# Kernel tuning notes

Hardware: AMD Instinct MI355X
Metric: run time of the kernel (lower is better)

The kernel has to match this reference:

```python
import jax, jax.numpy as jnp
import numpy as np

VOCAB = 8192
NT = 10        # spike encoder n_timesteps
N = 2048       # n_neurons
CA3 = 2048     # hippocampus CA3 size
S = 1024       # seq_len / context_length
SPARSITY = 0.05
LR = 0.01      # learning_rate * association_strength


def setup_inputs() -> dict:
    key = jax.random.key(0)
    k1, k2, k3, k4, k5 = jax.random.split(key, 5)
    token_ids = jax.random.randint(k1, (1, S), 0, VOCAB)                      # [batch=1, seq]
    sdr_table = jax.random.uniform(k2, (VOCAB, NT, N), dtype=jnp.float32)     # SDR encoder table
    pos_enc = jax.random.uniform(k3, (S, NT, N), dtype=jnp.float32)           # oscillatory position spikes (pre-threshold)
    w_hippo = jax.random.normal(k4, (CA3, N), dtype=jnp.float32) / np.sqrt(N).astype(np.float32)
    assoc_w = jax.random.normal(k5, (CA3, CA3), dtype=jnp.float32) * 0.01     # WEIGHT_INIT_SCALE_RECURRENT gaussian
    return {"token_ids": token_ids, "sdr_table": sdr_table, "pos_enc": pos_enc,
            "w_hippo": w_hippo, "assoc_w": assoc_w}


def reference(token_ids, sdr_table, pos_enc, w_hippo, assoc_w):
    """encode_sequence(learn=True): spike-encode each token, modulate by position
    spikes, run hippocampus, and sequentially Hebbian-update association weights.
    Returns final association weight matrix [CA3, CA3]."""
    tok_spikes = (sdr_table[token_ids[0]] < SPARSITY).astype(jnp.float32)
    # Position spikes (as_spikes=True -> binary) -> [S, NT, N]
    pos_spikes = (pos_enc < SPARSITY).astype(jnp.float32)
    # combined_spikes = token * (1 + 0.5 * position); sum over timesteps -> [S, N]
    hippo_input = (tok_spikes * (1.0 + 0.5 * pos_spikes)).sum(axis=1)
    # Hippocampus CA3 spikes: linear projection + threshold -> binary pattern [S, CA3]
    ca3_patterns = (hippo_input @ w_hippo.T > 0.0).astype(jnp.float32)

    # Sequential Hebbian association learning: W += lr * outer(post, pre), row-renorm.
    def step(W, pre_post):
        pre, post = pre_post
        W = W + LR * jnp.outer(post, pre)
        norm = jnp.maximum(jnp.linalg.norm(W, axis=1, keepdims=True), 1.0)
        return W / norm, None

    W_final, _ = jax.lax.scan(step, assoc_w, (ca3_patterns[:-1], ca3_patterns[1:]))
    return W_final
```

## Files before the change

### kernel.cpp

```cpp
#include <hip/hip_runtime.h>
#include <hip/hip_bf16.h>

#define NT    10
#define NN    2048
#define CA3C  2048
#define SEQ   1024
#define SPARS 0.05f
#define LRC   0.01f

typedef float          f32x4  __attribute__((ext_vector_type(4)));
typedef short          bf16x8 __attribute__((ext_vector_type(8)));
typedef unsigned short u16x4  __attribute__((ext_vector_type(4)));
typedef unsigned short u16x8  __attribute__((ext_vector_type(8)));

__device__ __forceinline__ unsigned short f2bf(float f) {
    unsigned u = __float_as_uint(f);
    u += 0x7FFFu + ((u >> 16) & 1u);
    return (unsigned short)(u >> 16);
}
__device__ __forceinline__ float bf2f(unsigned short h) {
    return __uint_as_float(((unsigned)h) << 16);
}

__device__ __forceinline__ void split8(const float* __restrict__ src,
        unsigned short* __restrict__ hi, unsigned short* __restrict__ lo, long blk) {
    long i = (blk * 256 + threadIdx.x) * 8;
    f32x4 x0 = *(const f32x4*)(src + i);
    f32x4 x1 = *(const f32x4*)(src + i + 4);
    float xs[8] = {x0.x, x0.y, x0.z, x0.w, x1.x, x1.y, x1.z, x1.w};
    u16x8 h, l;
    #pragma unroll
    for (int j = 0; j < 8; ++j) {
        unsigned short hb = f2bf(xs[j]);
        h[j] = hb;
        l[j] = f2bf(xs[j] - bf2f(hb));
    }
    *(u16x8*)(hi + i) = h;
    if (lo) *(u16x8*)(lo + i) = l;
}

__global__ __launch_bounds__(256) void k_front(const int* __restrict__ tok,
        const float* __restrict__ sdr, const float* __restrict__ pos,
        unsigned short* __restrict__ Hh, unsigned* __restrict__ cnt,
        const float* __restrict__ w_hippo, unsigned short* __restrict__ Wh,
        unsigned short* __restrict__ Wl, const float* __restrict__ assoc,
        unsigned short* __restrict__ Sh) {
    long id = blockIdx.x;
    if (id == 0 && threadIdx.x == 0) *cnt = 0;
    if (id < 2048) {
        int s = (int)(id >> 1);
        int n = ((int)(id & 1) * 256 + threadIdx.x) * 4;
        const float* sp = sdr + (long)tok[s] * (NT * NN) + n;
        const float* pp = pos + (long)s * (NT * NN) + n;
        float a0 = 0.f, a1 = 0.f, a2 = 0.f, a3 = 0.f;
        #pragma unroll
        for (int t = 0; t < NT; ++t) {
            float4 sv = *(const float4*)(sp + t * NN);
            float4 pv = *(const float4*)(pp + t * NN);
            if (sv.x < SPARS) a0 += (pv.x < SPARS) ? 1.5f : 1.0f;
            if (sv.y < SPARS) a1 += (pv.y < SPARS) ? 1.5f : 1.0f;
            if (sv.z < SPARS) a2 += (pv.z < SPARS) ? 1.5f : 1.0f;
            if (sv.w < SPARS) a3 += (pv.w < SPARS) ? 1.5f : 1.0f;
        }
        u16x4 o = { f2bf(a0), f2bf(a1), f2bf(a2), f2bf(a3) };
        *(u16x4*)(Hh + (long)s * NN + n) = o;
    } else {
        long b = id - 2048;
        if (b < 2048) split8(w_hippo, Wh, Wl, b);
        else          split8(assoc, Sh, nullptr, b - 2048);
    }
}

#define SPLIT_NONE 0
#define SPLIT_A    1
#define SPLIT_B    2

template<int MODE, int BN>
__global__ __launch_bounds__(256, 1) void k_mgemm(
        const unsigned short* __restrict__ A0, const unsigned short* __restrict__ A1,
        const unsigned short* __restrict__ Bh, const unsigned short* __restrict__ B1,
        float* __restrict__ C, int M, int N, int K,
        const float* __restrict__ Wadd, const float* __restrict__ af) {
    constexpr int NTW = BN / 32;
    constexpr int XR  = (MODE == SPLIT_A) ? 128 : BN;
    __shared__ unsigned short LA[128 * 70];
    __shared__ unsigned short LB[BN * 70];
    __shared__ unsigned short LX[(MODE == SPLIT_NONE) ? 70 : XR * 70];
    int tid = threadIdx.x, wid = tid >> 6, l = tid & 63;
    int m0 = blockIdx.y * 128, n0 = blockIdx.x * BN;
    int wr = wid >> 1, wc = wid & 1;
    int fr = l & 15, fk = l >> 4;
    f32x4 acc[4][NTW] = {};
    int srow = wid * 8 + (l >> 3);
    int scol = (l & 7) * 8;
    bf16x8 ra[4], rb[BN / 32], rx[XR / 32];
    #pragma unroll
    for (int i = 0; i < 4; ++i)
        ra[i] = *(const bf16x8*)(A0 + (long)(m0 + i * 32 + srow) * K + scol);
    #pragma unroll
    for (int i = 0; i < BN / 32; ++i)
        rb[i] = *(const bf16x8*)(Bh + (long)(n0 + i * 32 + srow) * K + scol);
    if (MODE == SPLIT_A)
        #pragma unroll
        for (int i = 0; i < XR / 32; ++i)
            rx[i] = *(const bf16x8*)(A1 + (long)(m0 + i * 32 + srow) * K + scol);
    if (MODE == SPLIT_B)
        #pragma unroll
        for (int i = 0; i < XR / 32; ++i)
            rx[i] = *(const bf16x8*)(B1 + (long)(n0 + i * 32 + srow) * K + scol);

    for (int k0 = 0; k0 < K; k0 += 64) {
        __syncthreads();
        #pragma unroll
        for (int i = 0; i < 4; ++i) *(bf16x8*)&LA[(i * 32 + srow) * 70 + scol] = ra[i];
        #pragma unroll
        for (int i = 0; i < BN / 32; ++i) *(bf16x8*)&LB[(i * 32 + srow) * 70 + scol] = rb[i];
        if (MODE != SPLIT_NONE)
            #pragma unroll
            for (int i = 0; i < XR / 32; ++i) *(bf16x8*)&LX[(i * 32 + srow) * 70 + scol] = rx[i];
        __syncthreads();
        if (k0 + 64 < K) {
            int kn = k0 + 64;
            #pragma unroll
            for (int i = 0; i < 4; ++i)
                ra[i] = *(const bf16x8*)(A0 + (long)(m0 + i * 32 + srow) * K + kn + scol);
            #pragma unroll
            for (int i = 0; i < BN / 32; ++i)
                rb[i] = *(const bf16x8*)(Bh + (long)(n0 + i * 32 + srow) * K + kn + scol);
            if (MODE == SPLIT_A)
                #pragma unroll
                for (int i = 0; i < XR / 32; ++i)
                    rx[i] = *(const bf16x8*)(A1 + (long)(m0 + i * 32 + srow) * K + kn + scol);
            if (MODE == SPLIT_B)
                #pragma unroll
                for (int i = 0; i < XR / 32; ++i)
                    rx[i] = *(const bf16x8*)(B1 + (long)(n0 + i * 32 + srow) * K + kn + scol);
        }
        #pragma unroll
        for (int ks = 0; ks < 2; ++ks) {
            bf16x8 av[4], bv[NTW], xv[4];
            #pragma unroll
            for (int t = 0; t < 4; ++t)
                av[t] = *(const bf16x8*)&LA[(wr * 64 + t * 16 + fr) * 70 + ks * 32 + fk * 8];
            #pragma unroll
            for (int t = 0; t < NTW; ++t)
                bv[t] = *(const bf16x8*)&LB[(wc * (BN / 2) + t * 16 + fr) * 70 + ks * 32 + fk * 8];
            if (MODE == SPLIT_A)
                #pragma unroll
                for (int t = 0; t < 4; ++t)
                    xv[t] = *(const bf16x8*)&LX[(wr * 64 + t * 16 + fr) * 70 + ks * 32 + fk * 8];
            if (MODE == SPLIT_B)
                #pragma unroll
                for (int t = 0; t < NTW; ++t)
                    xv[t] = *(const bf16x8*)&LX[(wc * (BN / 2) + t * 16 + fr) * 70 + ks * 32 + fk * 8];
            #pragma unroll
            for (int mt = 0; mt < 4; ++mt)
                #pragma unroll
                for (int nt = 0; nt < NTW; ++nt) {
                    acc[mt][nt] = __builtin_amdgcn_mfma_f32_16x16x32_bf16(av[mt], bv[nt], acc[mt][nt], 0, 0, 0);
                    if (MODE == SPLIT_A)
                        acc[mt][nt] = __builtin_amdgcn_mfma_f32_16x16x32_bf16(xv[mt], bv[nt], acc[mt][nt], 0, 0, 0);
                    if (MODE == SPLIT_B)
                        acc[mt][nt] = __builtin_amdgcn_mfma_f32_16x16x32_bf16(av[mt], xv[nt], acc[mt][nt], 0, 0, 0);
                }
        }
    }
    int drb = (l >> 4) * 4;
    #pragma unroll
    for (int mt = 0; mt < 4; ++mt)
        #pragma unroll
        for (int nt = 0; nt < NTW; ++nt)
            #pragma unroll
            for (int e = 0; e < 4; ++e) {
                int row = m0 + wr * 64 + mt * 16 + drb + e;
                int cc  = n0 + wc * (BN / 2) + nt * 16 + (l & 15);
                float v = acc[mt][nt][e];
                if (Wadd) v = fmaf(af[row], Wadd[(long)row * N + cc], v);
                C[(long)row * N + cc] = v;
            }
}

__global__ __launch_bounds__(256) void k_fixflag(const float* __restrict__ dots,
        unsigned* __restrict__ list, unsigned* __restrict__ cnt) {
    int i = blockIdx.x * 256 + threadIdx.x;
    int lane = threadIdx.x & 63;
    bool f = fabsf(dots[i]) < 1e-3f;
    unsigned long long m = __ballot(f);
    if (m == 0) return;
    unsigned b0 = 0;
    if (lane == 0) b0 = atomicAdd(cnt, (unsigned)__popcll(m));
    b0 = __shfl(b0, 0, 64);
    if (f) {
        unsigned rank = (unsigned)__popcll(m & ((1ull << lane) - 1ull));
        list[b0 + rank] = (unsigned)i;
    }
}

__global__ __launch_bounds__(64) void k_fix64(const unsigned* __restrict__ list,
        const unsigned* __restrict__ cnt, const unsigned short* __restrict__ Hh,
        const float* __restrict__ w, float* __restrict__ dots) {
    int lane = threadIdx.x;
    unsigned n = *cnt;
    for (unsigned idx = blockIdx.x; idx < n; idx += gridDim.x) {
        unsigned i = list[idx];
        int s = (int)(i >> 11), c = (int)(i & 2047);
        const unsigned short* hr = Hh + (long)s * NN;
        const float* wr = w + (long)c * NN;
        double a = 0.0;
        #pragma unroll
        for (int j = 0; j < 8; ++j) {
            int k = j * 256 + lane * 4;
            f32x4 wv = *(const f32x4*)(wr + k);
            u16x4 hv = *(const u16x4*)(hr + k);
            a += (double)bf2f(hv.x) * (double)wv.x + (double)bf2f(hv.y) * (double)wv.y
               + (double)bf2f(hv.z) * (double)wv.z + (double)bf2f(hv.w) * (double)wv.w;
        }
        #pragma unroll
        for (int o = 1; o < 64; o <<= 1) a += __shfl_xor(a, o, 64);
        if (lane == 0) dots[i] = (a > 0.0) ? 1.0f : -1.0f;
    }
}

__global__ __launch_bounds__(256) void k_packx(const float* __restrict__ dots,
        unsigned* __restrict__ preT, float* __restrict__ popf,
        unsigned short* __restrict__ Xb, unsigned* __restrict__ postT) {
    int wid = threadIdx.x >> 6, lane = threadIdx.x & 63;
    if (blockIdx.x < 256) {
        int s = blockIdx.x * 4 + wid;
        const float* row = dots + (long)s * CA3C + lane * 32;
        unsigned short* xrow = Xb + (long)s * CA3C + lane * 32;
        unsigned m = 0;
        #pragma unroll
        for (int j4 = 0; j4 < 8; ++j4) {
            f32x4 v = *(const f32x4*)(row + j4 * 4);
            u16x4 xb;
            xb.x = v.x > 0.f ? 0x3F80 : 0; xb.y = v.y > 0.f ? 0x3F80 : 0;
            xb.z = v.z > 0.f ? 0x3F80 : 0; xb.w = v.w > 0.f ? 0x3F80 : 0;
            m |= (v.x > 0.f ? 1u : 0u) << (j4 * 4 + 0);
            m |= (v.y > 0.f ? 1u : 0u) << (j4 * 4 + 1);
            m |= (v.z > 0.f ? 1u : 0u) << (j4 * 4 + 2);
            m |= (v.w > 0.f ? 1u : 0u) << (j4 * 4 + 3);
            *(u16x4*)(xrow + j4 * 4) = xb;
        }
        preT[lane * SEQ + s] = m;
        int pc = __popc(m);
        #pragma unroll
        for (int o = 1; o < 64; o <<= 1) pc += __shfl_xor(pc, o, 64);
        if (lane == 0) popf[s] = (float)pc;
    } else {
        __shared__ unsigned long long masks[4][64];
        int tile = (blockIdx.x - 256) * 4 + wid;
        int rg = tile & 31, sg = tile >> 5;
        int r0 = rg * 64;
        #pragma unroll 8
        for (int k = 0; k < 64; ++k) {
            int s = sg * 64 + k;
            float d = (s < SEQ - 1) ? dots[(long)(s + 1) * CA3C + r0 + lane] : -1.f;
            unsigned long long m = __ballot(d > 0.f);
            if (lane == 0) masks[wid][k] = m;
        }
        unsigned w0 = 0, w1 = 0;
        #pragma unroll
        for (int k = 0; k < 32; ++k) {
            w0 |= (unsigned)((masks[wid][k]      >> lane) & 1ull) << k;
            w1 |= (unsigned)((masks[wid][k + 32] >> lane) & 1ull) << k;
        }
        postT[(r0 + lane) * 32 + sg * 2]     = w0;
        postT[(r0 + lane) * 32 + sg * 2 + 1] = w1;
    }
}

__global__ __launch_bounds__(256) void k_transpose(const unsigned short* __restrict__ Xb,
        unsigned short* __restrict__ XbT) {
    __shared__ unsigned short t[64][72];
    int s0 = blockIdx.x * 64, n0 = blockIdx.y * 64;
    int tx = threadIdx.x & 63, ty = threadIdx.x >> 6;
    #pragma unroll
    for (int ii = 0; ii < 16; ++ii) {
        int i = ty + ii * 4;
        t[i][tx] = Xb[(long)(s0 + i) * CA3C + n0 + tx];
    }
    __syncthreads();
    #pragma unroll
    for (int ii = 0; ii < 16; ++ii) {
        int i = ty + ii * 4;
        XbT[(long)(n0 + i) * SEQ + s0 + tx] = t[tx][i];
    }
}

__global__ __launch_bounds__(256) void k_gram(const unsigned* __restrict__ preT,
        float* __restrict__ G, unsigned short* __restrict__ Gbh,
        unsigned short* __restrict__ Gbl) {
    int i = blockIdx.x;
    int t = threadIdx.x;
    int a0 = 0, a1 = 0, a2 = 0, a3 = 0;
    #pragma unroll 8
    for (int w = 0; w < 64; ++w) {
        unsigned ri = preT[w * SEQ + i];
        const unsigned* pr = preT + w * SEQ;
        a0 += __popc(ri & pr[t]);
        a1 += __popc(ri & pr[t + 256]);
        a2 += __popc(ri & pr[t + 512]);
        a3 += __popc(ri & pr[t + 768]);
    }
    long base = (long)i * SEQ;
    int vi[4] = {a0, a1, a2, a3};
    #pragma unroll
    for (int q = 0; q < 4; ++q) {
        long o = base + t + q * 256;
        float v = (float)vi[q];
        unsigned short h = f2bf(v);
        G[o] = v;
        Gbh[o] = h;
        Gbl[o] = f2bf(v - bf2f(h));
    }
}

__device__ __forceinline__ float wave_sum64(float x) {
    #define DPPADD(ctrl, rmask) \
        x += __int_as_float(__builtin_amdgcn_update_dpp(0, __float_as_int(x), ctrl, rmask, 0xF, true))
    DPPADD(0xB1, 0xF);
    DPPADD(0x4E, 0xF);
    DPPADD(0x141, 0xF);
    DPPADD(0x140, 0xF);
    DPPADD(0x142, 0xA);
    DPPADD(0x143, 0xC);
    #undef DPPADD
    return __int_as_float(__builtin_amdgcn_readlane(__float_as_int(x), 63));
}

__global__ __launch_bounds__(256) void k_scan2(const float* __restrict__ W0,
        const float* __restrict__ B0, const float* __restrict__ G,
        const unsigned short* __restrict__ Gbh, const unsigned short* __restrict__ Gbl,
        const unsigned* __restrict__ postT, const float* __restrict__ popf,
        unsigned short* __restrict__ Ch, unsigned short* __restrict__ Cl,
        float* __restrict__ alphaf) {
    __shared__ float Gd[64][68];
    __shared__ unsigned short BH[2][4096];
    __shared__ unsigned short BL[2][4096];
    __shared__ unsigned short CHL[8][1024];
    int tid = threadIdx.x, wid = tid >> 6, lane = tid & 63;
    int r = blockIdx.x * 4 + wid;
    int fr = lane & 15, fk = lane >> 4;
    int nl = tid >> 2, seg = tid & 3;
    const float* wr = W0 + (long)r * NN + lane * 32;
    f32x4 q0 = *(const f32x4*)(wr +  0), q1 = *(const f32x4*)(wr +  4);
    f32x4 q2 = *(const f32x4*)(wr +  8), q3 = *(const f32x4*)(wr + 12);
    f32x4 q4 = *(const f32x4*)(wr + 16), q5 = *(const f32x4*)(wr + 20);
    f32x4 q6 = *(const f32x4*)(wr + 24), q7 = *(const f32x4*)(wr + 28);
    f32x4 pp = q0*q0 + q1*q1 + q2*q2 + q3*q3 + q4*q4 + q5*q5 + q6*q6 + q7*q7;
    float nu = wave_sum64((pp.x + pp.y) + (pp.z + pp.w));
    float alpha = 1.f, inv_alpha = 1.f;
    { float t = fmaxf(nu, 1.f); alpha *= rsqrtf(t); inv_alpha *= sqrtf(t); nu = fminf(nu, 1.f); }
    float s0 = 1.f;

    bf16x8 ph0, ph1, pl0, pl1;
    for (int b = 0; b < 16; ++b) {
        __syncthreads();
        {
            const float* gs = G + (long)(b * 64 + nl) * SEQ + b * 64 + seg * 16;
            *(f32x4*)&Gd[nl][seg * 16 +  0] = *(const f32x4*)(gs +  0);
            *(f32x4*)&Gd[nl][seg * 16 +  4] = *(const f32x4*)(gs +  4);
            *(f32x4*)&Gd[nl][seg * 16 +  8] = *(const f32x4*)(gs +  8);
            *(f32x4*)&Gd[nl][seg * 16 + 12] = *(const f32x4*)(gs + 12);
        }
        if (b > 0) {
            const unsigned short* gh = Gbh + (long)(b * 64 + nl) * SEQ + seg * 16;
            const unsigned short* gl = Gbl + (long)(b * 64 + nl) * SEQ + seg * 16;
            ph0 = *(const bf16x8*)(gh); ph1 = *(const bf16x8*)(gh + 8);
            pl0 = *(const bf16x8*)(gl); pl1 = *(const bf16x8*)(gl + 8);
            *(bf16x8*)&BH[0][((seg * 2 + 0) * 64 + nl) * 8] = ph0;
            *(bf16x8*)&BH[0][((seg * 2 + 1) * 64 + nl) * 8] = ph1;
            *(bf16x8*)&BL[0][((seg * 2 + 0) * 64 + nl) * 8] = pl0;
            *(bf16x8*)&BL[0][((seg * 2 + 1) * 64 + nl) * 8] = pl1;
        }
        __syncthreads();
        f32x4 acc0 = {}, acc1 = {}, acc2 = {}, acc3 = {};
        for (int ch = 0; ch < b; ++ch) {
            if (ch + 1 < b) {
                const unsigned short* gh = Gbh + (long)(b * 64 + nl) * SEQ + (ch + 1) * 64 + seg * 16;
                const unsigned short* gl = Gbl + (long)(b * 64 + nl) * SEQ + (ch + 1) * 64 + seg * 16;
                ph0 = *(const bf16x8*)(gh); ph1 = *(const bf16x8*)(gh + 8);
                pl0 = *(const bf16x8*)(gl); pl1 = *(const bf16x8*)(gl + 8);
            }
            const unsigned short* bh = BH[ch & 1];
            const unsigned short* bl = BL[ch & 1];
            #pragma unroll
            for (int kt = 0; kt < 2; ++kt) {
                bf16x8 af = *(const bf16x8*)&CHL[fr & 7][ch * 64 + kt * 32 + fk * 8];
                #define MTILE(T, ACC) { \
                    bf16x8 vh = *(const bf16x8*)&bh[((kt * 4 + fk) * 64 + T * 16 + fr) * 8]; \
                    bf16x8 vl = *(const bf16x8*)&bl[((kt * 4 + fk) * 64 + T * 16 + fr) * 8]; \
                    ACC = __builtin_amdgcn_mfma_f32_16x16x32_bf16(af, vh, ACC, 0, 0, 0); \
                    ACC = __builtin_amdgcn_mfma_f32_16x16x32_bf16(af, vl, ACC, 0, 0, 0); }
                MTILE(0, acc0) MTILE(1, acc1) MTILE(2, acc2) MTILE(3, acc3)
                #undef MTILE
            }
            if (ch + 1 < b) {
                int nb = (ch + 1) & 1;
                *(bf16x8*)&BH[nb][((seg * 2 + 0) * 64 + nl) * 8] = ph0;
                *(bf16x8*)&BH[nb][((seg * 2 + 1) * 64 + nl) * 8] = ph1;
                *(bf16x8*)&BL[nb][((seg * 2 + 0) * 64 + nl) * 8] = pl0;
                *(bf16x8*)&BL[nb][((seg * 2 + 1) * 64 + nl) * 8] = pl1;
            }
            __syncthreads();
        }
        float t0 = (wid & 1) ? (acc0.z + acc0.w) : (acc0.x + acc0.y);
        float t1 = (wid & 1) ? (acc1.z + acc1.w) : (acc1.x + acc1.y);
        float t2 = (wid & 1) ? (acc2.z + acc2.w) : (acc2.x + acc2.y);
        float t3 = (wid & 1) ? (acc3.z + acc3.w) : (acc3.x + acc3.y);
        int sa = (((wid >> 1) * 16) + fr) * 4;
        float p0 = __int_as_float(__builtin_amdgcn_ds_bpermute(sa, __float_as_int(t0)));
        float p1 = __int_as_float(__builtin_amdgcn_ds_bpermute(sa, __float_as_int(t1)));
        float p2 = __int_as_float(__builtin_amdgcn_ds_bpermute(sa, __float_as_int(t2)));
        float p3 = __int_as_float(__builtin_amdgcn_ds_bpermute(sa, __float_as_int(t3)));
        float u = (fk == 0) ? p0 : (fk == 1) ? p1 : (fk == 2) ? p2 : p3;

        float myB0  = B0[(long)r * SEQ + b * 64 + lane];
        float mypop = popf[b * 64 + lane];
        unsigned long long pm;
        {   unsigned lo = postT[r * 32 + 2 * b], hi = postT[r * 32 + 2 * b + 1];
            pm = ((unsigned long long)(unsigned)__builtin_amdgcn_readfirstlane((int)hi) << 32)
               |  (unsigned long long)(unsigned)__builtin_amdgcn_readfirstlane((int)lo);
        }
        float dacc = fmaf(s0, myB0, u);
        float cj = 0.f;
        #pragma unroll
        for (int j = 0; j < 64; ++j) {
            if ((pm >> j) & 1ull) {
                float dot = __int_as_float(__builtin_amdgcn_readlane(__float_as_int(dacc), j));
                float pj  = __int_as_float(__builtin_amdgcn_readlane(__float_as_int(mypop), j));
                float c = LRC * inv_alpha;
                nu = fmaf(2.f * LRC, alpha * dot, fmaf(LRC * LRC, pj, nu));
                float t = fmaxf(nu, 1.f);
                alpha *= rsqrtf(t); inv_alpha *= sqrtf(t); nu = fminf(nu, 1.f);
                dacc = fmaf(c, Gd[j][lane], dacc);
                cj = (lane == j) ? c : cj;
            }
        }
        {   unsigned short hh = f2bf(cj);
            CHL[wid * 2 + 0][b * 64 + lane] = hh;
            CHL[wid * 2 + 1][b * 64 + lane] = f2bf(cj - bf2f(hh));
        }
        if (inv_alpha > 1e10f) {
            #pragma unroll 1
            for (int kk = 0; kk <= b; ++kk) {
                float v = (bf2f(CHL[wid * 2 + 0][kk * 64 + lane])
                         + bf2f(CHL[wid * 2 + 1][kk * 64 + lane])) * alpha;
                unsigned short hh = f2bf(v);
                CHL[wid * 2 + 0][kk * 64 + lane] = hh;
                CHL[wid * 2 + 1][kk * 64 + lane] = f2bf(v - bf2f(hh));
            }
            s0 *= alpha; alpha = 1.f; inv_alpha = 1.f;
        }
    }
    if (lane == 0) alphaf[r] = alpha * s0;
    #pragma unroll
    for (int kk = 0; kk < 16; ++kk) {
        float v = (bf2f(CHL[wid * 2 + 0][kk * 64 + lane])
                 + bf2f(CHL[wid * 2 + 1][kk * 64 + lane])) * alpha;
        unsigned short hh = f2bf(v);
        Ch[(long)r * SEQ + kk * 64 + lane] = hh;
        Cl[(long)r * SEQ + kk * 64 + lane] = f2bf(v - bf2f(hh));
    }
}

extern "C" void kernel_launch(void* const* d_in, const int* in_sizes, int n_in,
                              void* d_out, int out_size, void* d_ws, size_t ws_size,
                              hipStream_t stream) {
    const int*   tok     = (const int*)d_in[0];
    const float* sdr     = (const float*)d_in[1];
    const float* pos     = (const float*)d_in[2];
    const float* w_hippo = (const float*)d_in[3];
    const float* assoc   = (const float*)d_in[4];
    float* out = (float*)d_out;

    char* ws = (char*)d_ws;
    unsigned short* Hh  = (unsigned short*)(ws);
    float*          G   = (float*)(ws);
    unsigned short* Wh  = (unsigned short*)(ws + (4l << 20));
    unsigned short* Wl  = (unsigned short*)(ws + (12l << 20));
    float*          dots= (float*)(ws + (20l << 20));
    float*          B0f = dots;
    unsigned short* Xb  = (unsigned short*)(ws + (28l << 20));
    unsigned short* Gbh = Xb;
    unsigned short* Gbl = (unsigned short*)(ws + (30l << 20));
    unsigned short* XbT = (unsigned short*)(ws + (32l << 20));
    unsigned* preT   = (unsigned*)(ws + (36l << 20));
    unsigned* postT  = (unsigned*)(ws + (36l << 20) + 262144);
    float*    popf   = (float*)(ws + (36l << 20) + 524288);
    float*    alphaf = (float*)(ws + (36l << 20) + 532480);
    unsigned* cnt    = (unsigned*)(ws + (37l << 20));
    unsigned* list   = (unsigned*)(ws + (37l << 20) + 4096);
    unsigned short* Sh  = (unsigned short*)(ws + (40l << 20));
    unsigned short* Ch  = (unsigned short*)(ws + (48l << 20));
    unsigned short* Cl  = (unsigned short*)(ws + (52l << 20));

    k_front                <<<6144,         256, 0, stream>>>(tok, sdr, pos, Hh, cnt,
                                                              w_hippo, Wh, Wl, assoc, Sh);
    k_mgemm<SPLIT_B, 64>   <<<dim3(32, 8),  256, 0, stream>>>(Hh, nullptr, Wh, Wl, dots,
                                                              1024, 2048, 2048, nullptr, nullptr);
    k_fixflag              <<<8192,         256, 0, stream>>>(dots, list, cnt);
    k_fix64                <<<2048,          64, 0, stream>>>(list, cnt, Hh, w_hippo, dots);
    k_packx                <<<384,          256, 0, stream>>>(dots, preT, popf, Xb, postT);
    k_transpose            <<<dim3(16, 32), 256, 0, stream>>>(Xb, XbT);
    k_mgemm<SPLIT_NONE, 64><<<dim3(16, 16), 256, 0, stream>>>(Sh, nullptr, Xb, nullptr, B0f,
                                                              2048, 1024, 2048, nullptr, nullptr);
    k_gram                 <<<SEQ,          256, 0, stream>>>(preT, G, Gbh, Gbl);
    k_scan2                <<<512,          256, 0, stream>>>(assoc, B0f, G, Gbh, Gbl,
                                                              postT, popf, Ch, Cl, alphaf);
    k_mgemm<SPLIT_A, 128>  <<<dim3(16, 16), 256, 0, stream>>>(Ch, Cl, XbT, nullptr, out,
                                                              2048, 2048, 1024, assoc, alphaf);
}
```

Before: 459.8 us.

## Fuse flagging into GEMM epilogue and merge small kernels to cut launches

```diff
diff --git a/kernel.cpp b/kernel.cpp
--- a/kernel.cpp
+++ b/kernel.cpp
@@ -75,19 +75,19 @@
 #define SPLIT_A    1
 #define SPLIT_B    2
 
-template<int MODE, int BN>
-__global__ __launch_bounds__(256, 1) void k_mgemm(
+template<int MODE, int BN, int FLAG>
+__device__ __forceinline__ void mg_body(int bx, int by,
         const unsigned short* __restrict__ A0, const unsigned short* __restrict__ A1,
         const unsigned short* __restrict__ Bh, const unsigned short* __restrict__ B1,
         float* __restrict__ C, int M, int N, int K,
-        const float* __restrict__ Wadd, const float* __restrict__ af) {
+        const float* __restrict__ Wadd, const float* __restrict__ af,
+        unsigned* __restrict__ list, unsigned* __restrict__ cnt,
+        unsigned short* __restrict__ LA, unsigned short* __restrict__ LB,
+        unsigned short* __restrict__ LX) {
     constexpr int NTW = BN / 32;
     constexpr int XR  = (MODE == SPLIT_A) ? 128 : BN;
-    __shared__ unsigned short LA[128 * 70];
-    __shared__ unsigned short LB[BN * 70];
-    __shared__ unsigned short LX[(MODE == SPLIT_NONE) ? 70 : XR * 70];
     int tid = threadIdx.x, wid = tid >> 6, l = tid & 63;
-    int m0 = blockIdx.y * 128, n0 = blockIdx.x * BN;
+    int m0 = by * 128, n0 = bx * BN;
     int wr = wid >> 1, wc = wid & 1;
     int fr = l & 15, fk = l >> 4;
     f32x4 acc[4][NTW] = {};
@@ -177,22 +177,77 @@
                 float v = acc[mt][nt][e];
                 if (Wadd) v = fmaf(af[row], Wadd[(long)row * N + cc], v);
                 C[(long)row * N + cc] = v;
+                if (FLAG) {
+                    bool f = fabsf(v) < 1e-3f;
+                    unsigned long long mb = __ballot(f);
+                    if (mb) {
+                        unsigned base = 0;
+                        if (l == 0) base = atomicAdd(cnt, (unsigned)__popcll(mb));
+                        base = __shfl(base, 0, 64);
+                        if (f) {
+                            unsigned rank = (unsigned)__popcll(mb & ((1ull << l) - 1ull));
+                            list[base + rank] = (unsigned)((long)row * N + cc);
+                        }
+                    }
+                }
             }
 }
 
-__global__ __launch_bounds__(256) void k_fixflag(const float* __restrict__ dots,
+template<int MODE, int BN, int FLAG>
+__global__ __launch_bounds__(256, 1) void k_mgemm(
+        const unsigned short* __restrict__ A0, const unsigned short* __restrict__ A1,
+        const unsigned short* __restrict__ Bh, const unsigned short* __restrict__ B1,
+        float* __restrict__ C, int M, int N, int K,
+        const float* __restrict__ Wadd, const float* __restrict__ af,
         unsigned* __restrict__ list, unsigned* __restrict__ cnt) {
-    int i = blockIdx.x * 256 + threadIdx.x;
-    int lane = threadIdx.x & 63;
-    bool f = fabsf(dots[i]) < 1e-3f;
-    unsigned long long m = __ballot(f);
-    if (m == 0) return;
-    unsigned b0 = 0;
-    if (lane == 0) b0 = atomicAdd(cnt, (unsigned)__popcll(m));
-    b0 = __shfl(b0, 0, 64);
-    if (f) {
-        unsigned rank = (unsigned)__popcll(m & ((1ull << lane) - 1ull));
-        list[b0 + rank] = (unsigned)i;
+    constexpr int XR = (MODE == SPLIT_A) ? 128 : BN;
+    __shared__ unsigned short LA[128 * 70];
+    __shared__ unsigned short LB[BN * 70];
+    __shared__ unsigned short LX[(MODE == SPLIT_NONE) ? 70 : XR * 70];
+    mg_body<MODE, BN, FLAG>(blockIdx.x, blockIdx.y, A0, A1, Bh, B1, C, M, N, K,
+                            Wadd, af, list, cnt, LA, LB, LX);
+}
+
+__device__ __forceinline__ void gram_body(int i, const unsigned* __restrict__ preT,
+        float* __restrict__ G, unsigned short* __restrict__ Gbh,
+        unsigned short* __restrict__ Gbl) {
+    int t = threadIdx.x;
+    int a0 = 0, a1 = 0, a2 = 0, a3 = 0;
+    #pragma unroll 8
+    for (int w = 0; w < 64; ++w) {
+        unsigned ri = preT[w * SEQ + i];
+        const unsigned* pr = preT + w * SEQ;
+        a0 += __popc(ri & pr[t]);
+        a1 += __popc(ri & pr[t + 256]);
+        a2 += __popc(ri & pr[t + 512]);
+        a3 += __popc(ri & pr[t + 768]);
+    }
+    long base = (long)i * SEQ;
+    int vi[4] = {a0, a1, a2, a3};
+    #pragma unroll
+    for (int q = 0; q < 4; ++q) {
+        long o = base + t + q * 256;
+        float v = (float)vi[q];
+        unsigned short h = f2bf(v);
+        G[o] = v;
+        Gbh[o] = h;
+        Gbl[o] = f2bf(v - bf2f(h));
+    }
+}
+
+__global__ __launch_bounds__(256, 1) void k_mid(const unsigned short* __restrict__ Sh,
+        const unsigned short* __restrict__ Xb, float* __restrict__ B0f,
+        const unsigned* __restrict__ preT, float* __restrict__ G,
+        unsigned short* __restrict__ Gbh, unsigned short* __restrict__ Gbl) {
+    __shared__ unsigned short LA[128 * 70];
+    __shared__ unsigned short LB[64 * 70];
+    int id = blockIdx.x;
+    if (id < 256) {
+        mg_body<SPLIT_NONE, 64, 0>(id & 15, id >> 4, Sh, nullptr, Xb, nullptr, B0f,
+                                   2048, 1024, 2048, nullptr, nullptr, nullptr, nullptr,
+                                   LA, LB, LA);
+    } else {
+        gram_body(id - 256, preT, G, Gbh, Gbl);
     }
 }
 
@@ -223,7 +278,8 @@
 
 __global__ __launch_bounds__(256) void k_packx(const float* __restrict__ dots,
         unsigned* __restrict__ preT, float* __restrict__ popf,
-        unsigned short* __restrict__ Xb, unsigned* __restrict__ postT) {
+        unsigned short* __restrict__ Xb, unsigned* __restrict__ postT,
+        unsigned short* __restrict__ XbT) {
     int wid = threadIdx.x >> 6, lane = threadIdx.x & 63;
     if (blockIdx.x < 256) {
         int s = blockIdx.x * 4 + wid;
@@ -247,7 +303,7 @@
         #pragma unroll
         for (int o = 1; o < 64; o <<= 1) pc += __shfl_xor(pc, o, 64);
         if (lane == 0) popf[s] = (float)pc;
-    } else {
+    } else if (blockIdx.x < 384) {
         __shared__ unsigned long long masks[4][64];
         int tile = (blockIdx.x - 256) * 4 + wid;
         int rg = tile & 31, sg = tile >> 5;
@@ -267,52 +323,22 @@
         }
         postT[(r0 + lane) * 32 + sg * 2]     = w0;
         postT[(r0 + lane) * 32 + sg * 2 + 1] = w1;
-    }
-}
-
-__global__ __launch_bounds__(256) void k_transpose(const unsigned short* __restrict__ Xb,
-        unsigned short* __restrict__ XbT) {
-    __shared__ unsigned short t[64][72];
-    int s0 = blockIdx.x * 64, n0 = blockIdx.y * 64;
-    int tx = threadIdx.x & 63, ty = threadIdx.x >> 6;
-    #pragma unroll
-    for (int ii = 0; ii < 16; ++ii) {
-        int i = ty + ii * 4;
-        t[i][tx] = Xb[(long)(s0 + i) * CA3C + n0 + tx];
-    }
-    __syncthreads();
-    #pragma unroll
-    for (int ii = 0; ii < 16; ++ii) {
-        int i = ty + ii * 4;
-        XbT[(long)(n0 + i) * SEQ + s0 + tx] = t[tx][i];
-    }
-}
-
-__global__ __launch_bounds__(256) void k_gram(const unsigned* __restrict__ preT,
-        float* __restrict__ G, unsigned short* __restrict__ Gbh,
-        unsigned short* __restrict__ Gbl) {
-    int i = blockIdx.x;
-    int t = threadIdx.x;
-    int a0 = 0, a1 = 0, a2 = 0, a3 = 0;
-    #pragma unroll 8
-    for (int w = 0; w < 64; ++w) {
-        unsigned ri = preT[w * SEQ + i];
-        const unsigned* pr = preT + w * SEQ;
-        a0 += __popc(ri & pr[t]);
-        a1 += __popc(ri & pr[t + 256]);
-        a2 += __popc(ri & pr[t + 512]);
-        a3 += __popc(ri & pr[t + 768]);
-    }
-    long base = (long)i * SEQ;
-    int vi[4] = {a0, a1, a2, a3};
-    #pragma unroll
-    for (int q = 0; q < 4; ++q) {
-        long o = base + t + q * 256;
-        float v = (float)vi[q];
-        unsigned short h = f2bf(v);
-        G[o] = v;
-        Gbh[o] = h;
-        Gbl[o] = f2bf(v - bf2f(h));
+    } else {
+        __shared__ unsigned short t[64][72];
+        int tl = blockIdx.x - 384;
+        int s0 = (tl & 15) * 64, n0 = (tl >> 4) * 64;
+        int tx = threadIdx.x & 63, ty = threadIdx.x >> 6;
+        #pragma unroll
+        for (int ii = 0; ii < 16; ++ii) {
+            int i = ty + ii * 4;
+            t[i][tx] = (dots[(long)(s0 + i) * CA3C + n0 + tx] > 0.f) ? 0x3F80 : 0;
+        }
+        __syncthreads();
+        #pragma unroll
+        for (int ii = 0; ii < 16; ++ii) {
+            int i = ty + ii * 4;
+            XbT[(long)(n0 + i) * SEQ + s0 + tx] = t[tx][i];
+        }
     }
 }
 
@@ -483,8 +509,6 @@
     float*          dots= (float*)(ws + (20l << 20));
     float*          B0f = dots;
     unsigned short* Xb  = (unsigned short*)(ws + (28l << 20));
-    unsigned short* Gbh = Xb;
-    unsigned short* Gbl = (unsigned short*)(ws + (30l << 20));
     unsigned short* XbT = (unsigned short*)(ws + (32l << 20));
     unsigned* preT   = (unsigned*)(ws + (36l << 20));
     unsigned* postT  = (unsigned*)(ws + (36l << 20) + 262144);
@@ -495,20 +519,20 @@
     unsigned short* Sh  = (unsigned short*)(ws + (40l << 20));
     unsigned short* Ch  = (unsigned short*)(ws + (48l << 20));
     unsigned short* Cl  = (unsigned short*)(ws + (52l << 20));
-
-    k_front                <<<6144,         256, 0, stream>>>(tok, sdr, pos, Hh, cnt,
-                                                              w_hippo, Wh, Wl, assoc, Sh);
-    k_mgemm<SPLIT_B, 64>   <<<dim3(32, 8),  256, 0, stream>>>(Hh, nullptr, Wh, Wl, dots,
-                                                              1024, 2048, 2048, nullptr, nullptr);
-    k_fixflag              <<<8192,         256, 0, stream>>>(dots, list, cnt);
-    k_fix64                <<<2048,          64, 0, stream>>>(list, cnt, Hh, w_hippo, dots);
-    k_packx                <<<384,          256, 0, stream>>>(dots, preT, popf, Xb, postT);
-    k_transpose            <<<dim3(16, 32), 256, 0, stream>>>(Xb, XbT);
-    k_mgemm<SPLIT_NONE, 64><<<dim3(16, 16), 256, 0, stream>>>(Sh, nullptr, Xb, nullptr, B0f,
-                                                              2048, 1024, 2048, nullptr, nullptr);
-    k_gram                 <<<SEQ,          256, 0, stream>>>(preT, G, Gbh, Gbl);
-    k_scan2                <<<512,          256, 0, stream>>>(assoc, B0f, G, Gbh, Gbl,
-                                                              postT, popf, Ch, Cl, alphaf);
-    k_mgemm<SPLIT_A, 128>  <<<dim3(16, 16), 256, 0, stream>>>(Ch, Cl, XbT, nullptr, out,
-                                                              2048, 2048, 1024, assoc, alphaf);
-}
+    unsigned short* Gbh = (unsigned short*)(ws + (56l << 20));
+    unsigned short* Gbl = (unsigned short*)(ws + (58l << 20));
+
+    k_front                  <<<6144,         256, 0, stream>>>(tok, sdr, pos, Hh, cnt,
+                                                                w_hippo, Wh, Wl, assoc, Sh);
+    k_mgemm<SPLIT_B, 64, 1>  <<<dim3(32, 8),  256, 0, stream>>>(Hh, nullptr, Wh, Wl, dots,
+                                                                1024, 2048, 2048, nullptr, nullptr,
+                                                                list, cnt);
+    k_fix64                  <<<2048,          64, 0, stream>>>(list, cnt, Hh, w_hippo, dots);
+    k_packx                  <<<896,          256, 0, stream>>>(dots, preT, popf, Xb, postT, XbT);
+    k_mid                    <<<1280,         256, 0, stream>>>(Sh, Xb, B0f, preT, G, Gbh, Gbl);
+    k_scan2                  <<<512,          256, 0, stream>>>(assoc, B0f, G, Gbh, Gbl,
+                                                                postT, popf, Ch, Cl, alphaf);
+    k_mgemm<SPLIT_A, 128, 0> <<<dim3(16, 16), 256, 0, stream>>>(Ch, Cl, XbT, nullptr, out,
+                                                                2048, 2048, 1024, assoc, alphaf,
+                                                                nullptr, nullptr);
+}
```

After: 568.3 us. +23.6%, slower.
